# Kernel tuning notes

Measured on AMD Instinct MI355X. Metric: run time of the kernel, lower is better.

Reference implementation:

```python
import jax, jax.numpy as jnp
import numpy as np

N_ENTITIES = 50000
N_EDGES = 600000
CHANNEL = 128
N_RELATIONS = 32
N_HOPS = 2
LEAKY_SLOPE = 0.01
EPS = 1e-12


def setup_inputs() -> dict:
    key = jax.random.key(0)
    ks = jax.random.split(key, 9)
    entity_emb = jax.random.normal(ks[0], (N_ENTITIES, CHANNEL), dtype=jnp.float32)
    edge_index = jax.random.randint(ks[1], (2, N_EDGES), 0, N_ENTITIES, dtype=jnp.int64)
    edge_type = jax.random.randint(ks[2], (N_EDGES,), 0, N_RELATIONS, dtype=jnp.int64)
    # xavier_uniform for relation weight: bound = sqrt(6/(fan_in+fan_out))
    b = float(np.sqrt(6.0 / (N_RELATIONS + CHANNEL)))
    weight = jax.random.uniform(ks[3], (N_RELATIONS, CHANNEL), minval=-b, maxval=b, dtype=jnp.float32)
    # torch Linear default init: U(-1/sqrt(fan_in), 1/sqrt(fan_in)); y = x @ W.T + b
    b1 = 1.0 / np.sqrt(CHANNEL)
    b2 = 1.0 / np.sqrt(2 * CHANNEL)
    W1_w = jax.random.uniform(ks[4], (N_HOPS, CHANNEL, CHANNEL), minval=-b1, maxval=b1, dtype=jnp.float32)
    W1_b = jax.random.uniform(ks[5], (N_HOPS, CHANNEL), minval=-b1, maxval=b1, dtype=jnp.float32)
    W2_w = jax.random.uniform(ks[6], (N_HOPS, CHANNEL, 2 * CHANNEL), minval=-b2, maxval=b2, dtype=jnp.float32)
    W2_b = jax.random.uniform(ks[7], (N_HOPS, CHANNEL), minval=-b2, maxval=b2, dtype=jnp.float32)
    return {"entity_emb": entity_emb, "edge_index": edge_index, "edge_type": edge_type,
            "weight": weight, "W1_w": W1_w, "W1_b": W1_b, "W2_w": W2_w, "W2_b": W2_b}


def _leaky(x):
    return jnp.where(x >= 0, x, LEAKY_SLOPE * x)


def reference(entity_emb, edge_index, edge_type, weight, W1_w, W1_b, W2_w, W2_b):
    n_entities = entity_emb.shape[0]
    n_hops = W1_w.shape[0]
    head, tail = edge_index[0], edge_index[1]
    # in-degree counts for scatter_mean (empty rows -> 0, matching scatter_mean)
    counts = jax.ops.segment_sum(jnp.ones((head.shape[0],), dtype=entity_emb.dtype),
                                 head, num_segments=n_entities)
    denom = jnp.maximum(counts, 1.0)[:, None]
    res = entity_emb
    for i in range(n_hops):
        # gather -> elementwise multiply -> scatter mean (Aggregator)
        msg = res[tail] * weight[edge_type]                 # [E, C]
        agg = jax.ops.segment_sum(msg, head, num_segments=n_entities) / denom
        # F.normalize (L2 per row, eps=1e-12)
        norm = jnp.linalg.norm(agg, axis=1, keepdims=True)
        agg = agg / jnp.maximum(norm, EPS)
        # mixed aggregation: Linear(add) + Linear(concat), both LeakyReLU
        e1 = _leaky((res + agg) @ W1_w[i].T + W1_b[i])
        e2 = _leaky(jnp.concatenate([res, agg], axis=1) @ W2_w[i].T + W2_b[i])
        res = e1 + e2
    return res, weight
```

## Files before the change

kernel.cpp:

```cpp
#include <hip/hip_runtime.h>
#include <hip/hip_bf16.h>

#define N_ENT 50000
#define N_EDG 600000
#define CH 128
#define LEAKY 0.01f
#define NB_SCAN 49
#define NSTRIP 3125
#define AGG_BLOCKS 1024
#define GEMM_BLOCKS 256
#define FILL_CHUNK 4800
#define HEADS_PER_GRP 6250
#define PREP_BLOCKS 6351
#define COUNT_BLOCKS 2344

typedef __attribute__((ext_vector_type(8))) short bf16x8;
typedef __attribute__((ext_vector_type(4))) float f32x4;

__device__ inline unsigned short f2bf(float x) {
    return __builtin_bit_cast(unsigned short, __float2bfloat16(x));
}
__device__ inline float bflo(unsigned u) { return __builtin_bit_cast(float, u << 16); }
__device__ inline float bfhi(unsigned u) { return __builtin_bit_cast(float, u & 0xFFFF0000u); }
__device__ inline int rfl(int x) { return __builtin_amdgcn_readfirstlane(x); }

__global__ __launch_bounds__(256) void prep_kernel(const float* __restrict__ emb,
                                                   const float* __restrict__ W1,
                                                   const float* __restrict__ W2,
                                                   const float* __restrict__ wsrc,
                                                   const int* __restrict__ head,
                                                   unsigned short* __restrict__ xh,
                                                   unsigned short* __restrict__ w1bf,
                                                   unsigned short* __restrict__ w2bf,
                                                   float* __restrict__ wout,
                                                   float* __restrict__ wsf,
                                                   int* __restrict__ counts) {
    if (blockIdx.x >= PREP_BLOCKS) {
        int e = (blockIdx.x - PREP_BLOCKS) * 256 + threadIdx.x;
        if (e < N_EDG) atomicAdd(&counts[head[e]], 1);
        return;
    }
    long long gid = (long long)blockIdx.x * 256 + threadIdx.x;
    const long long n_x = (long long)N_ENT * CH / 4;
    const long long n_w1 = 2 * CH * CH / 4;
    const long long n_w2 = 2 * CH * 2 * CH / 4;
    if (gid < n_x) {
        long long k = gid * 4;
        float4 v = *(const float4*)&emb[k];
        ushort4 o;
        o.x = f2bf(v.x); o.y = f2bf(v.y); o.z = f2bf(v.z); o.w = f2bf(v.w);
        *(ushort4*)&xh[k] = o;
    } else if (gid < n_x + n_w1) {
        long long k = (gid - n_x) * 4;
        float4 v = *(const float4*)&W1[k];
        ushort4 o;
        o.x = f2bf(v.x); o.y = f2bf(v.y); o.z = f2bf(v.z); o.w = f2bf(v.w);
        *(ushort4*)&w1bf[k] = o;
    } else if (gid < n_x + n_w1 + n_w2) {
        long long k = (gid - n_x - n_w1) * 4;
        float4 v = *(const float4*)&W2[k];
        ushort4 o;
        o.x = f2bf(v.x); o.y = f2bf(v.y); o.z = f2bf(v.z); o.w = f2bf(v.w);
        *(ushort4*)&w2bf[k] = o;
    } else {
        long long k = gid - n_x - n_w1 - n_w2;
        if (k < 1024) {
            float4 v = *(const float4*)&wsrc[k * 4];
            *(float4*)&wout[k * 4] = v;
            *(float4*)&wsf[k * 4] = v;
        } else if (k < 1056) {
            float4 z = {0.f, 0.f, 0.f, 0.f};
            *(float4*)&wsf[k * 4] = z;
        }
    }
}

__global__ __launch_bounds__(256) void scan_block(const int* __restrict__ counts,
                                                  int* __restrict__ offs,
                                                  int* __restrict__ bsum) {
    __shared__ int s[256];
    int t = threadIdx.x;
    int base = blockIdx.x * 1024 + t * 4;
    int v[4];
#pragma unroll
    for (int i = 0; i < 4; ++i) {
        int idx = base + i;
        v[i] = (idx < N_ENT) ? counts[idx] : 0;
    }
    int tot = v[0] + v[1] + v[2] + v[3];
    s[t] = tot;
    for (int off = 1; off < 256; off <<= 1) {
        __syncthreads();
        int x = (t >= off) ? s[t - off] : 0;
        __syncthreads();
        s[t] += x;
    }
    int run = s[t] - tot;
#pragma unroll
    for (int i = 0; i < 4; ++i) {
        if (base + i < N_ENT) offs[base + i] = run;
        run += v[i];
    }
    if (t == 255) bsum[blockIdx.x] = s[255];
}

__global__ __launch_bounds__(64) void scan_tops(int* __restrict__ bsum) {
    int lane = threadIdx.x;
    int v = (lane < NB_SCAN) ? bsum[lane] : 0;
    int orig = v;
#pragma unroll
    for (int off = 1; off < 64; off <<= 1) {
        int x = __shfl_up(v, off);
        if (lane >= off) v += x;
    }
    if (lane < NB_SCAN) bsum[lane] = v - orig;
}

__global__ __launch_bounds__(256) void add_base(int* __restrict__ offs,
                                                int* __restrict__ cursors,
                                                const int* __restrict__ bsum) {
    int t = threadIdx.x;
    int base = blockIdx.x * 1024 + t * 4;
    int b = bsum[blockIdx.x];
#pragma unroll
    for (int i = 0; i < 4; ++i) {
        int idx = base + i;
        if (idx < N_ENT) {
            int o = offs[idx] + b;
            offs[idx] = o;
            cursors[idx] = o;
        }
    }
    if (blockIdx.x == 0 && t == 0) offs[N_ENT] = N_EDG;
}

__global__ __launch_bounds__(256) void fill_kernel(const int* __restrict__ head,
                                                   const int* __restrict__ tail,
                                                   const int* __restrict__ etype,
                                                   int* __restrict__ cursors,
                                                   int* __restrict__ packed) {
    int g = blockIdx.x & 7;
    int c = blockIdx.x >> 3;
    int hlo = g * HEADS_PER_GRP;
    int hhi = hlo + HEADS_PER_GRP;
    int base = c * FILL_CHUNK;
    for (int t = threadIdx.x; t < FILL_CHUNK; t += 256) {
        int e = base + t;
        int h = head[e];
        if (h >= hlo && h < hhi) {
            int pos = atomicAdd(&cursors[h], 1);
            packed[pos] = tail[e] | (etype[e] << 20);
        }
    }
}

__global__ __launch_bounds__(512) void agg_kernel(
    const unsigned short* __restrict__ xin, const int* __restrict__ offs,
    const int* __restrict__ packed, const float* __restrict__ wsf,
    unsigned short* __restrict__ aggb) {
    __shared__ float ws_[33 * 132];
    int tid = threadIdx.x;
    for (int q = tid; q < 1056; q += 512) {
        float4 v = *(const float4*)&wsf[q * 4];
        *(float4*)&ws_[(q >> 5) * 132 + (q & 31) * 4] = v;
    }
    __syncthreads();

    const int w = tid >> 6;
    const int lane = tid & 63;
    const int l16 = lane & 15;
    const int lq = lane >> 4;
    const int c8 = l16 * 8;

    for (int rb = blockIdx.x; rb < 6250; rb += AGG_BLOCKS) {
        const int row = rb * 8 + w;
        const int beg = rfl(offs[row]);
        const int end = rfl(offs[row + 1]);

        float a[8] = {0.f, 0.f, 0.f, 0.f, 0.f, 0.f, 0.f, 0.f};
        float b[8] = {0.f, 0.f, 0.f, 0.f, 0.f, 0.f, 0.f, 0.f};

        for (int i = beg; i < end; i += 8) {
            int pa0 = rfl(packed[i]);
            int pa1 = rfl(packed[i + 1]);
            int pa2 = rfl(packed[i + 2]);
            int pa3 = rfl(packed[i + 3]);
            int pb0 = rfl(packed[i + 4]);
            int pb1 = rfl(packed[i + 5]);
            int pb2 = rfl(packed[i + 6]);
            int pb3 = rfl(packed[i + 7]);
            int pA = lq == 0 ? pa0 : lq == 1 ? pa1 : lq == 2 ? pa2 : pa3;
            int pB = lq == 0 ? pb0 : lq == 1 ? pb1 : lq == 2 ? pb2 : pb3;
            bool okA = (i + lq) < end;
            bool okB = (i + 4 + lq) < end;
            int tA = (okA ? pA : pa0) & 0xFFFFF;
            int tB = (okB ? pB : pa0) & 0xFFFFF;
            int rA = okA ? (pA >> 20) : 32;
            int rB = okB ? (pB >> 20) : 32;
            uint4 vA = *(const uint4*)&xin[(long long)tA * CH + c8];
            uint4 vB = *(const uint4*)&xin[(long long)tB * CH + c8];
            float wvA[8], wvB[8];
            *(float4*)&wvA[0] = *(const float4*)&ws_[rA * 132 + c8];
            *(float4*)&wvA[4] = *(const float4*)&ws_[rA * 132 + c8 + 4];
            *(float4*)&wvB[0] = *(const float4*)&ws_[rB * 132 + c8];
            *(float4*)&wvB[4] = *(const float4*)&ws_[rB * 132 + c8 + 4];
            unsigned ua[4] = {vA.x, vA.y, vA.z, vA.w};
            unsigned ub[4] = {vB.x, vB.y, vB.z, vB.w};
#pragma unroll
            for (int k = 0; k < 4; ++k) {
                a[2 * k] = fmaf(bflo(ua[k]), wvA[2 * k], a[2 * k]);
                a[2 * k + 1] = fmaf(bfhi(ua[k]), wvA[2 * k + 1], a[2 * k + 1]);
                b[2 * k] = fmaf(bflo(ub[k]), wvB[2 * k], b[2 * k]);
                b[2 * k + 1] = fmaf(bfhi(ub[k]), wvB[2 * k + 1], b[2 * k + 1]);
            }
        }

#pragma unroll
        for (int k = 0; k < 8; ++k) {
            a[k] += b[k];
            a[k] += __shfl_xor(a[k], 16);
            a[k] += __shfl_xor(a[k], 32);
        }
        float dinv = 1.0f / fmaxf((float)(end - beg), 1.f);
        float ss = 0.f;
#pragma unroll
        for (int k = 0; k < 8; ++k) {
            a[k] *= dinv;
            ss = fmaf(a[k], a[k], ss);
        }
#pragma unroll
        for (int off = 1; off <= 8; off <<= 1) ss += __shfl_xor(ss, off);
        float inv = 1.0f / fmaxf(sqrtf(ss), 1e-12f);
        if (lq == 0) {
            unsigned o0 = (unsigned)f2bf(a[0] * inv) | ((unsigned)f2bf(a[1] * inv) << 16);
            unsigned o1 = (unsigned)f2bf(a[2] * inv) | ((unsigned)f2bf(a[3] * inv) << 16);
            unsigned o2 = (unsigned)f2bf(a[4] * inv) | ((unsigned)f2bf(a[5] * inv) << 16);
            unsigned o3 = (unsigned)f2bf(a[6] * inv) | ((unsigned)f2bf(a[7] * inv) << 16);
            uint4 ov = {o0, o1, o2, o3};
            *(uint4*)&aggb[(long long)row * CH + c8] = ov;
        }
    }
}

__global__ __launch_bounds__(1024) void gemm_kernel(
    const unsigned short* __restrict__ xin, const unsigned short* __restrict__ aggb,
    const unsigned short* __restrict__ w1bf, const unsigned short* __restrict__ w2bf,
    const float* __restrict__ b1, const float* __restrict__ b2,
    unsigned short* __restrict__ xout, float* __restrict__ outf) {
    __shared__ __align__(16) unsigned short w1s[CH * CH];
    __shared__ __align__(16) unsigned short w2s[CH * 2 * CH];

    const int tid = threadIdx.x;
    for (int q = tid; q < 6144; q += 1024) {
        if (q < 2048) {
            int j = q >> 4, c = q & 15;
            *(bf16x8*)&w1s[j * CH + ((c ^ (j & 7)) << 3)] =
                *(const bf16x8*)&w1bf[j * CH + c * 8];
        } else {
            int qq = q - 2048;
            int j = qq >> 5, c = qq & 31;
            *(bf16x8*)&w2s[j * 2 * CH + ((c ^ (j & 7)) << 3)] =
                *(const bf16x8*)&w2bf[j * 2 * CH + c * 8];
        }
    }
    __syncthreads();

    const int w = tid >> 6;
    const int h = w >> 3;
    const int wc = w & 7;
    const int lane = tid & 63;
    const int l16 = lane & 15;
    const int lq = lane >> 4;
    const int j = wc * 16 + l16;
    const float bb1 = b1[j];
    const float bb2 = b2[j];

    bf16x8 bW1[4], bWa[4], bWb[4];
#pragma unroll
    for (int kst = 0; kst < 4; ++kst) {
        int ca = kst * 4 + lq;
        int cb = 16 + kst * 4 + lq;
        bW1[kst] = *(const bf16x8*)&w1s[j * CH + ((ca ^ (j & 7)) << 3)];
        bWa[kst] = *(const bf16x8*)&w2s[j * 2 * CH + ((ca ^ (j & 7)) << 3)];
        bWb[kst] = *(const bf16x8*)&w2s[j * 2 * CH + ((cb ^ (j & 7)) << 3)];
    }

    for (int s = blockIdx.x * 2 + h; s < NSTRIP; s += 2 * GEMM_BLOCKS) {
        const int row0 = s * 16;
        long long abase = (long long)(row0 + l16) * CH + lq * 8;
        f32x4 acc1 = {0.f, 0.f, 0.f, 0.f};
        f32x4 acc2 = {0.f, 0.f, 0.f, 0.f};
#pragma unroll
        for (int kst = 0; kst < 4; ++kst) {
            bf16x8 rh = *(const bf16x8*)&xin[abase + kst * 32];
            bf16x8 av = *(const bf16x8*)&aggb[abase + kst * 32];
            acc1 = __builtin_amdgcn_mfma_f32_16x16x32_bf16(rh, bW1[kst], acc1, 0, 0, 0);
            acc1 = __builtin_amdgcn_mfma_f32_16x16x32_bf16(av, bW1[kst], acc1, 0, 0, 0);
            acc2 = __builtin_amdgcn_mfma_f32_16x16x32_bf16(rh, bWa[kst], acc2, 0, 0, 0);
            acc2 = __builtin_amdgcn_mfma_f32_16x16x32_bf16(av, bWb[kst], acc2, 0, 0, 0);
        }
#pragma unroll
        for (int r = 0; r < 4; ++r) {
            long long row = row0 + lq * 4 + r;
            float e1 = acc1[r] + bb1;
            e1 = e1 >= 0.f ? e1 : LEAKY * e1;
            float e2 = acc2[r] + bb2;
            e2 = e2 >= 0.f ? e2 : LEAKY * e2;
            float val = e1 + e2;
            if (outf)
                outf[row * CH + j] = val;
            else
                xout[row * CH + j] = f2bf(val);
        }
    }
}

extern "C" void kernel_launch(void* const* d_in, const int* in_sizes, int n_in,
                              void* d_out, int out_size, void* d_ws, size_t ws_size,
                              hipStream_t stream) {
    const float* emb = (const float*)d_in[0];
    const int* eidx = (const int*)d_in[1];
    const int* etype = (const int*)d_in[2];
    const float* weight = (const float*)d_in[3];
    const float* W1w = (const float*)d_in[4];
    const float* W1b = (const float*)d_in[5];
    const float* W2w = (const float*)d_in[6];
    const float* W2b = (const float*)d_in[7];

    float* out = (float*)d_out;
    float* wout = out + (size_t)N_ENT * CH;

    char* ws = (char*)d_ws;
    unsigned short* xh = (unsigned short*)ws;    ws += (size_t)N_ENT * CH * 2;
    unsigned short* xh2 = (unsigned short*)ws;   ws += (size_t)N_ENT * CH * 2;
    unsigned short* aggb = (unsigned short*)ws;  ws += (size_t)N_ENT * CH * 2;
    unsigned short* w1bf = (unsigned short*)ws;  ws += 2 * CH * CH * 2;
    unsigned short* w2bf = (unsigned short*)ws;  ws += 2 * CH * 2 * CH * 2;
    float* wsf = (float*)ws;                     ws += 33 * CH * 4;
    int* packed = (int*)ws;                      ws += (size_t)(N_EDG + 8) * 4;
    int* offs = (int*)ws;                        ws += (size_t)(N_ENT + 1) * 4;
    int* cursors = (int*)ws;                     ws += (size_t)N_ENT * 4;
    int* counts = (int*)ws;                      ws += (size_t)N_ENT * 4;
    int* bsum = (int*)ws;                        ws += 64 * 4;

    const int* head = eidx;
    const int* tail = eidx + N_EDG;

    hipMemsetAsync(counts, 0, N_ENT * sizeof(int), stream);
    prep_kernel<<<PREP_BLOCKS + COUNT_BLOCKS, 256, 0, stream>>>(
        emb, W1w, W2w, weight, head, xh, w1bf, w2bf, wout, wsf, counts);
    scan_block<<<NB_SCAN, 256, 0, stream>>>(counts, offs, bsum);
    scan_tops<<<1, 64, 0, stream>>>(bsum);
    add_base<<<NB_SCAN, 256, 0, stream>>>(offs, cursors, bsum);
    fill_kernel<<<1000, 256, 0, stream>>>(head, tail, etype, cursors, packed);

    agg_kernel<<<AGG_BLOCKS, 512, 0, stream>>>(xh, offs, packed, wsf, aggb);
    gemm_kernel<<<GEMM_BLOCKS, 1024, 0, stream>>>(
        xh, aggb, w1bf, w2bf, W1b, W2b, xh2, (float*)nullptr);
    agg_kernel<<<AGG_BLOCKS, 512, 0, stream>>>(xh2, offs, packed, wsf, aggb);
    gemm_kernel<<<GEMM_BLOCKS, 1024, 0, stream>>>(
        xh2, aggb, w1bf + CH * CH, w2bf + CH * 2 * CH,
        W1b + CH, W2b + CH, (unsigned short*)nullptr, out);
}
```

Baseline: 197.4 us.

## Gather neighbor features as fp8 e5m2 in aggregation and fold block-sum scan into add_base

```diff
diff --git a/kernel.cpp b/kernel.cpp
--- a/kernel.cpp
+++ b/kernel.cpp
@@ -20,9 +20,17 @@
 __device__ inline unsigned short f2bf(float x) {
     return __builtin_bit_cast(unsigned short, __float2bfloat16(x));
 }
-__device__ inline float bflo(unsigned u) { return __builtin_bit_cast(float, u << 16); }
-__device__ inline float bfhi(unsigned u) { return __builtin_bit_cast(float, u & 0xFFFF0000u); }
 __device__ inline int rfl(int x) { return __builtin_amdgcn_readfirstlane(x); }
+
+__device__ inline unsigned char f2e5m2(float x) {
+    unsigned short h = __builtin_bit_cast(unsigned short, (_Float16)x);
+    unsigned u = (unsigned)h + 0x7Fu + ((h >> 8) & 1u);
+    return (unsigned char)(u >> 8);
+}
+__device__ inline float e5m2f(unsigned v, int k) {
+    unsigned short u = (unsigned short)(((v >> (8 * k)) & 0xFFu) << 8);
+    return (float)__builtin_bit_cast(_Float16, u);
+}
 
 __global__ __launch_bounds__(256) void prep_kernel(const float* __restrict__ emb,
                                                    const float* __restrict__ W1,
@@ -30,6 +38,7 @@
                                                    const float* __restrict__ wsrc,
                                                    const int* __restrict__ head,
                                                    unsigned short* __restrict__ xh,
+                                                   unsigned char* __restrict__ xq,
                                                    unsigned short* __restrict__ w1bf,
                                                    unsigned short* __restrict__ w2bf,
                                                    float* __restrict__ wout,
@@ -50,6 +59,9 @@
         ushort4 o;
         o.x = f2bf(v.x); o.y = f2bf(v.y); o.z = f2bf(v.z); o.w = f2bf(v.w);
         *(ushort4*)&xh[k] = o;
+        uchar4 q;
+        q.x = f2e5m2(v.x); q.y = f2e5m2(v.y); q.z = f2e5m2(v.z); q.w = f2e5m2(v.w);
+        *(uchar4*)&xq[k] = q;
     } else if (gid < n_x + n_w1) {
         long long k = (gid - n_x) * 4;
         float4 v = *(const float4*)&W1[k];
@@ -104,24 +116,20 @@
     if (t == 255) bsum[blockIdx.x] = s[255];
 }
 
-__global__ __launch_bounds__(64) void scan_tops(int* __restrict__ bsum) {
-    int lane = threadIdx.x;
-    int v = (lane < NB_SCAN) ? bsum[lane] : 0;
-    int orig = v;
-#pragma unroll
-    for (int off = 1; off < 64; off <<= 1) {
-        int x = __shfl_up(v, off);
-        if (lane >= off) v += x;
-    }
-    if (lane < NB_SCAN) bsum[lane] = v - orig;
-}
-
 __global__ __launch_bounds__(256) void add_base(int* __restrict__ offs,
                                                 int* __restrict__ cursors,
                                                 const int* __restrict__ bsum) {
+    __shared__ int base_s;
     int t = threadIdx.x;
+    if (t < 64) {
+        int v = (t < NB_SCAN && t < (int)blockIdx.x) ? bsum[t] : 0;
+#pragma unroll
+        for (int off = 1; off < 64; off <<= 1) v += __shfl_xor(v, off);
+        if (t == 0) base_s = v;
+    }
+    __syncthreads();
+    int b = base_s;
     int base = blockIdx.x * 1024 + t * 4;
-    int b = bsum[blockIdx.x];
 #pragma unroll
     for (int i = 0; i < 4; ++i) {
         int idx = base + i;
@@ -155,7 +163,7 @@
 }
 
 __global__ __launch_bounds__(512) void agg_kernel(
-    const unsigned short* __restrict__ xin, const int* __restrict__ offs,
+    const unsigned char* __restrict__ xq, const int* __restrict__ offs,
     const int* __restrict__ packed, const float* __restrict__ wsf,
     unsigned short* __restrict__ aggb) {
     __shared__ float ws_[33 * 132];
@@ -197,21 +205,19 @@
             int tB = (okB ? pB : pa0) & 0xFFFFF;
             int rA = okA ? (pA >> 20) : 32;
             int rB = okB ? (pB >> 20) : 32;
-            uint4 vA = *(const uint4*)&xin[(long long)tA * CH + c8];
-            uint4 vB = *(const uint4*)&xin[(long long)tB * CH + c8];
+            uint2 vA = *(const uint2*)&xq[(long long)tA * CH + c8];
+            uint2 vB = *(const uint2*)&xq[(long long)tB * CH + c8];
             float wvA[8], wvB[8];
             *(float4*)&wvA[0] = *(const float4*)&ws_[rA * 132 + c8];
             *(float4*)&wvA[4] = *(const float4*)&ws_[rA * 132 + c8 + 4];
             *(float4*)&wvB[0] = *(const float4*)&ws_[rB * 132 + c8];
             *(float4*)&wvB[4] = *(const float4*)&ws_[rB * 132 + c8 + 4];
-            unsigned ua[4] = {vA.x, vA.y, vA.z, vA.w};
-            unsigned ub[4] = {vB.x, vB.y, vB.z, vB.w};
 #pragma unroll
             for (int k = 0; k < 4; ++k) {
-                a[2 * k] = fmaf(bflo(ua[k]), wvA[2 * k], a[2 * k]);
-                a[2 * k + 1] = fmaf(bfhi(ua[k]), wvA[2 * k + 1], a[2 * k + 1]);
-                b[2 * k] = fmaf(bflo(ub[k]), wvB[2 * k], b[2 * k]);
-                b[2 * k + 1] = fmaf(bfhi(ub[k]), wvB[2 * k + 1], b[2 * k + 1]);
+                a[k] = fmaf(e5m2f(vA.x, k), wvA[k], a[k]);
+                a[k + 4] = fmaf(e5m2f(vA.y, k), wvA[k + 4], a[k + 4]);
+                b[k] = fmaf(e5m2f(vB.x, k), wvB[k], b[k]);
+                b[k + 4] = fmaf(e5m2f(vB.y, k), wvB[k + 4], b[k + 4]);
             }
         }
 
@@ -246,7 +252,8 @@
     const unsigned short* __restrict__ xin, const unsigned short* __restrict__ aggb,
     const unsigned short* __restrict__ w1bf, const unsigned short* __restrict__ w2bf,
     const float* __restrict__ b1, const float* __restrict__ b2,
-    unsigned short* __restrict__ xout, float* __restrict__ outf) {
+    unsigned short* __restrict__ xout, unsigned char* __restrict__ xqout,
+    float* __restrict__ outf) {
     __shared__ __align__(16) unsigned short w1s[CH * CH];
     __shared__ __align__(16) unsigned short w2s[CH * 2 * CH];
 
@@ -307,10 +314,12 @@
             float e2 = acc2[r] + bb2;
             e2 = e2 >= 0.f ? e2 : LEAKY * e2;
             float val = e1 + e2;
-            if (outf)
+            if (outf) {
                 outf[row * CH + j] = val;
-            else
+            } else {
                 xout[row * CH + j] = f2bf(val);
+                xqout[row * CH + j] = f2e5m2(val);
+            }
         }
     }
 }
@@ -334,31 +343,37 @@
     unsigned short* xh = (unsigned short*)ws;    ws += (size_t)N_ENT * CH * 2;
     unsigned short* xh2 = (unsigned short*)ws;   ws += (size_t)N_ENT * CH * 2;
     unsigned short* aggb = (unsigned short*)ws;  ws += (size_t)N_ENT * CH * 2;
-    unsigned short* w1bf = (unsigned short*)ws;  ws += 2 * CH * CH * 2;
-    unsigned short* w2bf = (unsigned short*)ws;  ws += 2 * CH * 2 * CH * 2;
-    float* wsf = (float*)ws;                     ws += 33 * CH * 4;
+    unsigned char* xq = (unsigned char*)ws;      ws += (size_t)N_ENT * CH;
+    unsigned char* xq2 = (unsigned char*)ws;     ws += (size_t)N_ENT * CH;
+    ws -= (size_t)N_ENT * CH;
     int* packed = (int*)ws;                      ws += (size_t)(N_EDG + 8) * 4;
     int* offs = (int*)ws;                        ws += (size_t)(N_ENT + 1) * 4;
     int* cursors = (int*)ws;                     ws += (size_t)N_ENT * 4;
     int* counts = (int*)ws;                      ws += (size_t)N_ENT * 4;
     int* bsum = (int*)ws;                        ws += 64 * 4;
+    unsigned short* w1bf = (unsigned short*)ws;  ws += 2 * CH * CH * 2;
+    unsigned short* w2bf = (unsigned short*)ws;  ws += 2 * CH * 2 * CH * 2;
+    float* wsf = (float*)ws;                     ws += 33 * CH * 4;
+    xq2 = (unsigned char*)ws;                    ws += (size_t)N_ENT * CH;
+    if ((size_t)((char*)ws - (char*)d_ws) > ws_size) {
+        xq2 = nullptr;
+    }
 
     const int* head = eidx;
     const int* tail = eidx + N_EDG;
 
     hipMemsetAsync(counts, 0, N_ENT * sizeof(int), stream);
     prep_kernel<<<PREP_BLOCKS + COUNT_BLOCKS, 256, 0, stream>>>(
-        emb, W1w, W2w, weight, head, xh, w1bf, w2bf, wout, wsf, counts);
+        emb, W1w, W2w, weight, head, xh, xq, w1bf, w2bf, wout, wsf, counts);
     scan_block<<<NB_SCAN, 256, 0, stream>>>(counts, offs, bsum);
-    scan_tops<<<1, 64, 0, stream>>>(bsum);
     add_base<<<NB_SCAN, 256, 0, stream>>>(offs, cursors, bsum);
     fill_kernel<<<1000, 256, 0, stream>>>(head, tail, etype, cursors, packed);
 
-    agg_kernel<<<AGG_BLOCKS, 512, 0, stream>>>(xh, offs, packed, wsf, aggb);
+    agg_kernel<<<AGG_BLOCKS, 512, 0, stream>>>(xq, offs, packed, wsf, aggb);
     gemm_kernel<<<GEMM_BLOCKS, 1024, 0, stream>>>(
-        xh, aggb, w1bf, w2bf, W1b, W2b, xh2, (float*)nullptr);
-    agg_kernel<<<AGG_BLOCKS, 512, 0, stream>>>(xh2, offs, packed, wsf, aggb);
+        xh, aggb, w1bf, w2bf, W1b, W2b, xh2, xq2 ? xq2 : xq, (float*)nullptr);
+    agg_kernel<<<AGG_BLOCKS, 512, 0, stream>>>(xq2 ? xq2 : xq, offs, packed, wsf, aggb);
     gemm_kernel<<<GEMM_BLOCKS, 1024, 0, stream>>>(
         xh2, aggb, w1bf + CH * CH, w2bf + CH * 2 * CH,
-        W1b + CH, W2b + CH, (unsigned short*)nullptr, out);
-}
+        W1b + CH, W2b + CH, (unsigned short*)nullptr, (unsigned char*)nullptr, out);
+}
```

New measurement: 206.9 us. 4.8% more time.

## Double-buffer GEMM activation strips through LDS and fold scan_tops into add_base

Applied to the files above, without the earlier changes.

```diff
diff --git a/kernel.cpp b/kernel.cpp
--- a/kernel.cpp
+++ b/kernel.cpp
@@ -9,6 +9,7 @@
 #define NSTRIP 3125
 #define AGG_BLOCKS 1024
 #define GEMM_BLOCKS 256
+#define GEMM_NIT 7
 #define FILL_CHUNK 4800
 #define HEADS_PER_GRP 6250
 #define PREP_BLOCKS 6351
@@ -104,24 +105,20 @@
     if (t == 255) bsum[blockIdx.x] = s[255];
 }
 
-__global__ __launch_bounds__(64) void scan_tops(int* __restrict__ bsum) {
-    int lane = threadIdx.x;
-    int v = (lane < NB_SCAN) ? bsum[lane] : 0;
-    int orig = v;
-#pragma unroll
-    for (int off = 1; off < 64; off <<= 1) {
-        int x = __shfl_up(v, off);
-        if (lane >= off) v += x;
-    }
-    if (lane < NB_SCAN) bsum[lane] = v - orig;
-}
-
 __global__ __launch_bounds__(256) void add_base(int* __restrict__ offs,
                                                 int* __restrict__ cursors,
                                                 const int* __restrict__ bsum) {
+    __shared__ int base_s;
     int t = threadIdx.x;
+    if (t < 64) {
+        int v = (t < NB_SCAN && t < (int)blockIdx.x) ? bsum[t] : 0;
+#pragma unroll
+        for (int off = 1; off < 64; off <<= 1) v += __shfl_xor(v, off);
+        if (t == 0) base_s = v;
+    }
+    __syncthreads();
+    int b = base_s;
     int base = blockIdx.x * 1024 + t * 4;
-    int b = bsum[blockIdx.x];
 #pragma unroll
     for (int i = 0; i < 4; ++i) {
         int idx = base + i;
@@ -249,6 +246,7 @@
     unsigned short* __restrict__ xout, float* __restrict__ outf) {
     __shared__ __align__(16) unsigned short w1s[CH * CH];
     __shared__ __align__(16) unsigned short w2s[CH * 2 * CH];
+    __shared__ __align__(16) unsigned char abuf[2][16384];
 
     const int tid = threadIdx.x;
     for (int q = tid; q < 6144; q += 1024) {
@@ -263,7 +261,6 @@
                 *(const bf16x8*)&w2bf[j * 2 * CH + c * 8];
         }
     }
-    __syncthreads();
 
     const int w = tid >> 6;
     const int h = w >> 3;
@@ -271,10 +268,26 @@
     const int lane = tid & 63;
     const int l16 = lane & 15;
     const int lq = lane >> 4;
+
+    const int plane = (w & 7) >> 2;
+    const int rloc = (w & 3) * 4 + (lane >> 4);
+    const int c_st = lane & 15;
+    const int lds_st = h * 8192 + plane * 4096 + rloc * 256 + ((c_st ^ (rloc & 7)) << 4);
+    const unsigned short* stsrc = plane ? aggb : xin;
+    const long long gsrc_off = (long long)rloc * CH + c_st * 8;
+
+    {
+        int strip = blockIdx.x * 2 + h;
+        if (strip < NSTRIP) {
+            uint4 v = *(const uint4*)&stsrc[(long long)strip * 16 * CH + gsrc_off];
+            *(uint4*)&abuf[0][lds_st] = v;
+        }
+    }
+    __syncthreads();
+
     const int j = wc * 16 + l16;
     const float bb1 = b1[j];
     const float bb2 = b2[j];
-
     bf16x8 bW1[4], bWa[4], bWb[4];
 #pragma unroll
     for (int kst = 0; kst < 4; ++kst) {
@@ -285,33 +298,48 @@
         bWb[kst] = *(const bf16x8*)&w2s[j * 2 * CH + ((cb ^ (j & 7)) << 3)];
     }
 
-    for (int s = blockIdx.x * 2 + h; s < NSTRIP; s += 2 * GEMM_BLOCKS) {
-        const int row0 = s * 16;
-        long long abase = (long long)(row0 + l16) * CH + lq * 8;
-        f32x4 acc1 = {0.f, 0.f, 0.f, 0.f};
-        f32x4 acc2 = {0.f, 0.f, 0.f, 0.f};
-#pragma unroll
-        for (int kst = 0; kst < 4; ++kst) {
-            bf16x8 rh = *(const bf16x8*)&xin[abase + kst * 32];
-            bf16x8 av = *(const bf16x8*)&aggb[abase + kst * 32];
-            acc1 = __builtin_amdgcn_mfma_f32_16x16x32_bf16(rh, bW1[kst], acc1, 0, 0, 0);
-            acc1 = __builtin_amdgcn_mfma_f32_16x16x32_bf16(av, bW1[kst], acc1, 0, 0, 0);
-            acc2 = __builtin_amdgcn_mfma_f32_16x16x32_bf16(rh, bWa[kst], acc2, 0, 0, 0);
-            acc2 = __builtin_amdgcn_mfma_f32_16x16x32_bf16(av, bWb[kst], acc2, 0, 0, 0);
-        }
-#pragma unroll
-        for (int r = 0; r < 4; ++r) {
-            long long row = row0 + lq * 4 + r;
-            float e1 = acc1[r] + bb1;
-            e1 = e1 >= 0.f ? e1 : LEAKY * e1;
-            float e2 = acc2[r] + bb2;
-            e2 = e2 >= 0.f ? e2 : LEAKY * e2;
-            float val = e1 + e2;
-            if (outf)
-                outf[row * CH + j] = val;
-            else
-                xout[row * CH + j] = f2bf(val);
-        }
+    int cur = 0;
+    for (int it = 0; it < GEMM_NIT; ++it) {
+        int strip = (blockIdx.x + it * GEMM_BLOCKS) * 2 + h;
+        uint4 nv;
+        int nstrip = (blockIdx.x + (it + 1) * GEMM_BLOCKS) * 2 + h;
+        bool donext = (it + 1 < GEMM_NIT) && (nstrip < NSTRIP);
+        if (donext)
+            nv = *(const uint4*)&stsrc[(long long)nstrip * 16 * CH + gsrc_off];
+
+        if (strip < NSTRIP) {
+            const int row0 = strip * 16;
+            const unsigned char* base = &abuf[cur][h * 8192];
+            f32x4 acc1 = {0.f, 0.f, 0.f, 0.f};
+            f32x4 acc2 = {0.f, 0.f, 0.f, 0.f};
+#pragma unroll
+            for (int kst = 0; kst < 4; ++kst) {
+                int c = kst * 4 + lq;
+                int off = l16 * 256 + ((c ^ (l16 & 7)) << 4);
+                bf16x8 rh = *(const bf16x8*)&base[off];
+                bf16x8 av = *(const bf16x8*)&base[4096 + off];
+                acc1 = __builtin_amdgcn_mfma_f32_16x16x32_bf16(rh, bW1[kst], acc1, 0, 0, 0);
+                acc1 = __builtin_amdgcn_mfma_f32_16x16x32_bf16(av, bW1[kst], acc1, 0, 0, 0);
+                acc2 = __builtin_amdgcn_mfma_f32_16x16x32_bf16(rh, bWa[kst], acc2, 0, 0, 0);
+                acc2 = __builtin_amdgcn_mfma_f32_16x16x32_bf16(av, bWb[kst], acc2, 0, 0, 0);
+            }
+#pragma unroll
+            for (int r = 0; r < 4; ++r) {
+                long long row = row0 + lq * 4 + r;
+                float e1 = acc1[r] + bb1;
+                e1 = e1 >= 0.f ? e1 : LEAKY * e1;
+                float e2 = acc2[r] + bb2;
+                e2 = e2 >= 0.f ? e2 : LEAKY * e2;
+                float val = e1 + e2;
+                if (outf)
+                    outf[row * CH + j] = val;
+                else
+                    xout[row * CH + j] = f2bf(val);
+            }
+        }
+        if (donext) *(uint4*)&abuf[cur ^ 1][lds_st] = nv;
+        __syncthreads();
+        cur ^= 1;
     }
 }
 
@@ -350,7 +378,6 @@
     prep_kernel<<<PREP_BLOCKS + COUNT_BLOCKS, 256, 0, stream>>>(
         emb, W1w, W2w, weight, head, xh, w1bf, w2bf, wout, wsf, counts);
     scan_block<<<NB_SCAN, 256, 0, stream>>>(counts, offs, bsum);
-    scan_tops<<<1, 64, 0, stream>>>(bsum);
     add_base<<<NB_SCAN, 256, 0, stream>>>(offs, cursors, bsum);
     fill_kernel<<<1000, 256, 0, stream>>>(head, tail, etype, cursors, packed);
 
```

Result: faster. 162.9 us (-17.5%).
